# Kernel optimization log

Measured on AMD Instinct MI355X. Metric: run time of the kernel, lower is better.

The kernel has to match this reference:

```python
import jax, jax.numpy as jnp
import numpy as np

B, C_IN, T, IMG, P = 4, 3, 8, 224, 16
E, DEPTH, D_INNER, N_ST, DT_R, K = 384, 24, 768, 16, 24, 4
HP = IMG // P
NP_ = HP * HP          # 196 patches per frame
L = T * NP_            # 1568 tokens
EPS = 1e-5


def setup_inputs():
    key = jax.random.key(0)
    ks = jax.random.split(key, 24)
    r = lambda k, s, sc=0.02: jax.random.normal(k, s, jnp.float32) * sc
    inp = {
        "x": jax.random.normal(ks[0], (B, C_IN, T, IMG, IMG), jnp.float32),
        "patch_w": r(ks[1], (E, C_IN, 1, P, P)),
        "patch_b": jnp.zeros((E,), jnp.float32),
        "pos_embed": r(ks[2], (NP_, E)),
        "temporal_pos": r(ks[3], (T, E)),
        "imp_w1": r(ks[4], (E, E)),
        "imp_b1": jnp.zeros((E,), jnp.float32),
        "imp_w2": r(ks[5], (1, E)),
        "imp_b2": jnp.zeros((1,), jnp.float32),
        "in_w": r(ks[6], (DEPTH, 2 * D_INNER, E)),
        "out_w": r(ks[7], (DEPTH, E, D_INNER)),
        "norm_w": jnp.ones((DEPTH, E), jnp.float32),
        "norm_f_w": jnp.ones((E,), jnp.float32),
    }
    A_row = jnp.log(jnp.arange(1, N_ST + 1, dtype=jnp.float32))  # S4D-real init
    for i, sfx in enumerate(["", "_b"]):
        b = 8 + 4 * i
        inp["conv_w" + sfx] = r(ks[b], (DEPTH, D_INNER, K), 0.1)
        inp["conv_b" + sfx] = jnp.zeros((DEPTH, D_INNER), jnp.float32)
        inp["xp_w" + sfx] = r(ks[b + 1], (DEPTH, DT_R + 2 * N_ST, D_INNER))
        inp["dt_w" + sfx] = r(ks[b + 2], (DEPTH, D_INNER, DT_R), 0.01)
        inp["dt_b" + sfx] = jax.random.uniform(ks[b + 3], (DEPTH, D_INNER), jnp.float32, -4.6, -2.3)
        inp["A_log" + sfx] = jnp.tile(A_row, (DEPTH, D_INNER, 1))
        inp["D" + sfx] = jnp.ones((DEPTH, D_INNER), jnp.float32)
    return inp


def rmsnorm(x, w):
    x = x.astype(jnp.float32)
    return x * jax.lax.rsqrt(jnp.mean(x * x, axis=-1, keepdims=True) + EPS) * w


def causal_conv1d(x, w, b):
    # x: [B,L,D]; depthwise causal conv with kernel K
    xt = x.transpose(0, 2, 1)  # B D L
    y = jax.lax.conv_general_dilated(
        xt, w[:, None, :], (1,), [(K - 1, 0)],
        dimension_numbers=("NCH", "OIH", "NCH"), feature_group_count=D_INNER)
    return (y + b[None, :, None]).transpose(0, 2, 1)


def selective_scan(xt, dt, Bm, Cm, A, Dp):
    # xt,dt: [B,L,D]; Bm,Cm: [B,L,N]; A: [D,N]
    def step(h, ins):
        dt_t, x_t, B_t, C_t = ins  # [B,D],[B,D],[B,N],[B,N]
        h = h * jnp.exp(dt_t[..., None] * A) + (dt_t * x_t)[..., None] * B_t[:, None, :]
        return h, jnp.einsum('bdn,bn->bd', h, C_t)
    h0 = jnp.zeros((xt.shape[0], D_INNER, N_ST), xt.dtype)
    xs = (dt.transpose(1, 0, 2), xt.transpose(1, 0, 2),
          Bm.transpose(1, 0, 2), Cm.transpose(1, 0, 2))
    _, ys = jax.lax.scan(step, h0, xs)
    return ys.transpose(1, 0, 2) + xt * Dp


def mamba_dir(xc, z, cw, cb, xpw, dtw, dtb, Alog, Dp):
    xt = jax.nn.silu(causal_conv1d(xc, cw, cb))
    dbc = jnp.einsum('bld,ed->ble', xt, xpw)
    dt_low = dbc[..., :DT_R]
    Bm = dbc[..., DT_R:DT_R + N_ST]
    Cm = dbc[..., DT_R + N_ST:]
    dt = jax.nn.softplus(jnp.einsum('blr,dr->bld', dt_low, dtw) + dtb)
    y = selective_scan(xt, dt, Bm, Cm, -jnp.exp(Alog), Dp)
    return y * jax.nn.silu(z)


def mamba_block(h, p):
    xz = jnp.einsum('ble,fe->blf', h, p['in_w'])
    xc, z = xz[..., :D_INNER], xz[..., D_INNER:]
    yf = mamba_dir(xc, z, p['conv_w'], p['conv_b'], p['xp_w'], p['dt_w'], p['dt_b'], p['A_log'], p['D'])
    flip = lambda t: t[:, ::-1, :]
    yb = flip(mamba_dir(flip(xc), flip(z), p['conv_w_b'], p['conv_b_b'], p['xp_w_b'],
                        p['dt_w_b'], p['dt_b_b'], p['A_log_b'], p['D_b']))
    return jnp.einsum('bld,ed->ble', yf + yb, p['out_w'])


def _encoder(x, patch_w, patch_b, pos_embed, temporal_pos, imp_w1, imp_b1, imp_w2, imp_b2,
             in_w, out_w, norm_w, norm_f_w,
             conv_w, conv_b, xp_w, dt_w, dt_b, A_log, D,
             conv_w_b, conv_b_b, xp_w_b, dt_w_b, dt_b_b, A_log_b, D_b, mixer=mamba_block):
    Bn = x.shape[0]
    # PatchEmbed: Conv3d kernel (1,P,P) stride (1,P,P) == patchify + matmul
    xp = x.reshape(Bn, C_IN, T, HP, P, HP, P)
    xp = xp.transpose(0, 2, 3, 5, 1, 4, 6).reshape(Bn, T, NP_, C_IN * P * P)
    tok = xp @ patch_w.reshape(E, C_IN * P * P).T + patch_b  # [B,T,N,E]
    tok = tok + pos_embed[None, None] + temporal_pos[None, :, None, :]
    xseq = tok.reshape(Bn, L, E)
    # token importance gating
    h1 = jax.nn.relu(xseq @ imp_w1.T + imp_b1)
    logits = (h1 @ imp_w2.T + imp_b2)[..., 0]  # [B,L]
    xseq = xseq * jax.nn.sigmoid(logits)[..., None]
    stacked = {'in_w': in_w, 'out_w': out_w, 'norm_w': norm_w,
               'conv_w': conv_w, 'conv_b': conv_b, 'xp_w': xp_w, 'dt_w': dt_w,
               'dt_b': dt_b, 'A_log': A_log, 'D': D,
               'conv_w_b': conv_w_b, 'conv_b_b': conv_b_b, 'xp_w_b': xp_w_b,
               'dt_w_b': dt_w_b, 'dt_b_b': dt_b_b, 'A_log_b': A_log_b, 'D_b': D_b}

    def layer_fn(carry, p):
        hidden, residual = carry
        residual = (hidden + residual).astype(jnp.float32)  # fused add-norm, prenorm
        hn = rmsnorm(residual, p['norm_w'])
        hidden = mixer(hn, p)
        return (hidden, residual), None

    (hidden, residual), _ = jax.lax.scan(layer_fn, (xseq, jnp.zeros_like(xseq)), stacked)
    feats = rmsnorm(hidden + residual, norm_f_w)
    return feats, logits


def reference(x, patch_w, patch_b, pos_embed, temporal_pos, imp_w1, imp_b1, imp_w2, imp_b2,
              in_w, out_w, norm_w, norm_f_w,
              conv_w, conv_b, xp_w, dt_w, dt_b, A_log, D,
              conv_w_b, conv_b_b, xp_w_b, dt_w_b, dt_b_b, A_log_b, D_b):
    return _encoder(x, patch_w, patch_b, pos_embed, temporal_pos, imp_w1, imp_b1, imp_w2, imp_b2,
                    in_w, out_w, norm_w, norm_f_w,
                    conv_w, conv_b, xp_w, dt_w, dt_b, A_log, D,
                    conv_w_b, conv_b_b, xp_w_b, dt_w_b, dt_b_b, A_log_b, D_b)
```

## Files before the change

kernel.cpp:

```cpp
#include <hip/hip_runtime.h>
#include <hip/hip_bf16.h>

#define LL 1568
#define EE 384
#define DD 768
#define BB 4

typedef float f32x4 __attribute__((ext_vector_type(4)));
typedef unsigned short u16x2 __attribute__((ext_vector_type(2)));
typedef unsigned short u16x4 __attribute__((ext_vector_type(4)));
typedef unsigned short u16x8 __attribute__((ext_vector_type(8)));
typedef __bf16 bf16x8 __attribute__((ext_vector_type(8)));

__device__ inline unsigned short f2bf(float f) {
    unsigned int u = __builtin_bit_cast(unsigned int, f);
    u += 0x7fffu + ((u >> 16) & 1u);
    return (unsigned short)(u >> 16);
}
__device__ inline float bf2f(unsigned short u) {
    unsigned int v = ((unsigned int)u) << 16;
    return __builtin_bit_cast(float, v);
}
__device__ inline float silu_f(float v) { return v / (1.f + __expf(-v)); }
__device__ inline float exp2_f(float v) { return __builtin_amdgcn_exp2f(v); }

__global__ __launch_bounds__(256) void k_cvt(const float* __restrict__ src,
                                             unsigned short* __restrict__ dst, int n4) {
    int i = blockIdx.x * 256 + threadIdx.x;
    int stride = gridDim.x * 256;
    for (; i < n4; i += stride) {
        f32x4 v = *(const f32x4*)(src + (size_t)i * 4);
        u16x4 o;
#pragma unroll
        for (int j = 0; j < 4; j++) o[j] = f2bf(v[j]);
        *(u16x4*)(dst + (size_t)i * 4) = o;
    }
}

__global__ __launch_bounds__(256) void k_pad_xpw(const float* __restrict__ src,
                                                 unsigned short* __restrict__ dst) {
    const int total = 24 * 64 * 768;
    for (int i = blockIdx.x * 256 + threadIdx.x; i < total; i += gridDim.x * 256) {
        int l = i / (64 * 768);
        int r = (i / 768) % 64;
        int dcol = i % 768;
        dst[i] = (r < 56) ? f2bf(src[((size_t)l * 56 + r) * 768 + dcol]) : (unsigned short)0;
    }
}

__global__ __launch_bounds__(256) void k_pad_dtw(const float* __restrict__ src,
                                                 unsigned short* __restrict__ dst) {
    const int total = 24 * 768 * 32;
    for (int i = blockIdx.x * 256 + threadIdx.x; i < total; i += gridDim.x * 256) {
        int kk = i & 31;
        int nrow = i >> 5;
        dst[i] = (kk < 24) ? f2bf(src[(size_t)nrow * 24 + kk]) : (unsigned short)0;
    }
}

__global__ __launch_bounds__(256) void k_patch(const float* __restrict__ x,
                                               unsigned short* __restrict__ patches) {
    int bid = blockIdx.x;
    int b = bid / LL, rr = bid % LL, t = rr / 196, pp = rr % 196, hp = pp / 14, wp = pp % 14;
    for (int k = threadIdx.x; k < 768; k += 256) {
        int c = k >> 8, rem = k & 255, i = rem >> 4, j = rem & 15;
        patches[(size_t)bid * 768 + k] =
            f2bf(x[(((size_t)(b * 3 + c) * 8 + t) * 224 + hp * 16 + i) * 224 + wp * 16 + j]);
    }
}

template <int EPI, bool ASUM, bool OUTBF>
__global__ __launch_bounds__(256) void k_gemm(
    const unsigned short* __restrict__ A, const unsigned short* __restrict__ A2,
    const unsigned short* __restrict__ W, const unsigned short* __restrict__ W2,
    float* __restrict__ C, unsigned short* __restrict__ Cb, int K, int ldc,
    const float* __restrict__ bias, const float* __restrict__ bias2,
    const float* __restrict__ pos, const float* __restrict__ tpos) {
    const int tid = threadIdx.x;
    const int m0 = blockIdx.y * 128;
    const int n0 = blockIdx.x * 128;
    __shared__ unsigned short As[128 * 40];
    __shared__ unsigned short Ws[128 * 40];
    const int sr = tid >> 2;
    const int skc = tid & 3;

    const unsigned short* Wp = W;
    const float* biasp = bias;
    if constexpr (EPI == 3) {
        if (m0 >= 6272) { Wp = W2; biasp = bias2; }
    }

    f32x4 acc[4][4];
#pragma unroll
    for (int mi = 0; mi < 4; mi++)
#pragma unroll
        for (int ni = 0; ni < 4; ni++) acc[mi][ni] = (f32x4){0.f, 0.f, 0.f, 0.f};

    const int lane = tid & 63;
    const int wv = tid >> 6;
    const int wm = (wv & 1) << 6;
    const int wn = (wv >> 1) << 6;
    const int lr = lane & 15;
    const int kg = lane >> 4;

    u16x8 ar[2], wr_[2];
    auto loadT = [&](int kt) {
#pragma unroll
        for (int i = 0; i < 2; i++) {
            size_t ka = (size_t)(m0 + sr + 64 * i) * K + kt * 32 + skc * 8;
            u16x8 v = *(const u16x8*)(A + ka);
            if constexpr (ASUM) {
                u16x8 v2 = *(const u16x8*)(A2 + ka);
#pragma unroll
                for (int j = 0; j < 8; j++) v[j] = f2bf(bf2f(v[j]) + bf2f(v2[j]));
            }
            ar[i] = v;
            wr_[i] = *(const u16x8*)(Wp + (size_t)(n0 + sr + 64 * i) * K + kt * 32 + skc * 8);
        }
    };

    const int nK = K >> 5;
    loadT(0);
    for (int kt = 0; kt < nK; ++kt) {
#pragma unroll
        for (int i = 0; i < 2; i++) {
            *(u16x8*)&As[(sr + 64 * i) * 40 + skc * 8] = ar[i];
            *(u16x8*)&Ws[(sr + 64 * i) * 40 + skc * 8] = wr_[i];
        }
        __syncthreads();
        if (kt + 1 < nK) loadT(kt + 1);
        bf16x8 af[4], bfm[4];
#pragma unroll
        for (int mi = 0; mi < 4; mi++)
            af[mi] = *(const bf16x8*)&As[(wm + mi * 16 + lr) * 40 + kg * 8];
#pragma unroll
        for (int ni = 0; ni < 4; ni++)
            bfm[ni] = *(const bf16x8*)&Ws[(wn + ni * 16 + lr) * 40 + kg * 8];
#pragma unroll
        for (int mi = 0; mi < 4; mi++)
#pragma unroll
            for (int ni = 0; ni < 4; ni++)
                acc[mi][ni] = __builtin_amdgcn_mfma_f32_16x16x32_bf16(af[mi], bfm[ni], acc[mi][ni], 0, 0, 0);
        __syncthreads();
    }

#pragma unroll
    for (int mi = 0; mi < 4; mi++)
#pragma unroll
        for (int ni = 0; ni < 4; ni++)
#pragma unroll
            for (int j = 0; j < 4; j++) {
                int m = m0 + wm + mi * 16 + kg * 4 + j;
                int n = n0 + wn + ni * 16 + lr;
                float v = acc[mi][ni][j];
                if constexpr (EPI == 1) {
                    int rr = m % LL;
                    int t = rr / 196, p = rr % 196;
                    v += bias[n] + pos[p * EE + n] + tpos[t * EE + n];
                    C[(size_t)m * ldc + n] = v;
                    Cb[(size_t)m * ldc + n] = f2bf(v);
                } else if constexpr (EPI == 2) {
                    v += bias[n];
                    v = fmaxf(v, 0.f);
                    C[(size_t)m * ldc + n] = v;
                } else if constexpr (EPI == 3) {
                    v += biasp[n];
                    float sp = (v > 20.f) ? v : log1pf(__expf(v));
                    Cb[(size_t)m * ldc + n] = f2bf(sp);
                } else {
                    if constexpr (OUTBF)
                        Cb[(size_t)m * ldc + n] = f2bf(v);
                    else
                        C[(size_t)m * ldc + n] = v;
                }
            }
}

__global__ __launch_bounds__(64) void k_logits(const float* __restrict__ h1, const float* __restrict__ w2,
                                               const float* __restrict__ b2, float* __restrict__ xseq,
                                               float* __restrict__ logits_out) {
    int row = blockIdx.x;
    int lane = threadIdx.x;
    float acc = 0.f;
#pragma unroll
    for (int i = 0; i < 6; i++) {
        int e = lane + i * 64;
        acc += h1[(size_t)row * EE + e] * w2[e];
    }
#pragma unroll
    for (int off = 32; off >= 1; off >>= 1) acc += __shfl_xor(acc, off);
    float logit = acc + b2[0];
    if (lane == 0) logits_out[row] = logit;
    float sg = 1.f / (1.f + __expf(-logit));
#pragma unroll
    for (int i = 0; i < 6; i++) {
        int e = lane + i * 64;
        xseq[(size_t)row * EE + e] *= sg;
    }
}

template <bool OBF>
__global__ __launch_bounds__(256) void k_norm(const float* __restrict__ hidden, float* __restrict__ resid,
                                              const float* __restrict__ wn, float* __restrict__ outf,
                                              unsigned short* __restrict__ outb,
                                              int first, int writeResid) {
    int row = blockIdx.x * 4 + (threadIdx.x >> 6);
    int lane = threadIdx.x & 63;
    size_t base = (size_t)row * EE;
    float v[6];
    float ss = 0.f;
#pragma unroll
    for (int i = 0; i < 6; i++) {
        int e = lane + i * 64;
        float h = hidden[base + e];
        float r = first ? 0.f : resid[base + e];
        float s = h + r;
        v[i] = s;
        ss += s * s;
    }
#pragma unroll
    for (int off = 32; off >= 1; off >>= 1) ss += __shfl_xor(ss, off);
    if (writeResid) {
#pragma unroll
        for (int i = 0; i < 6; i++) resid[base + lane + i * 64] = v[i];
    }
    float sc = rsqrtf(ss * (1.f / 384.f) + 1e-5f);
#pragma unroll
    for (int i = 0; i < 6; i++) {
        int e = lane + i * 64;
        float o = v[i] * sc * wn[e];
        if constexpr (OBF)
            outb[base + e] = f2bf(o);
        else
            outf[base + e] = o;
    }
}

__global__ __launch_bounds__(256) void k_conv(
    const unsigned short* __restrict__ xz,
    const float* __restrict__ cw_f, const float* __restrict__ cb_f,
    const float* __restrict__ cw_b, const float* __restrict__ cb_b,
    unsigned short* __restrict__ xtb) {
    const int tid = threadIdx.x;
    if (tid >= 192) return;
    const int b = blockIdx.y, dir = blockIdx.z;
    const float* cw = dir ? cw_b : cw_f;
    const float* cb = dir ? cb_b : cb_f;
    const int o = tid % 96, tg = tid / 96;
    const int t0 = blockIdx.x * 16 + tg * 8;
    const int d0 = o * 8;
    const size_t xzb = (size_t)b * LL * 1536;
    const size_t obase = ((size_t)dir * BB + b) * LL;

    f32x4 wq[8];
    float bv[8];
#pragma unroll
    for (int j = 0; j < 8; j++) {
        wq[j] = *(const f32x4*)&cw[(d0 + j) * 4];
        bv[j] = cb[d0 + j];
    }

    auto loadrow = [&](int t) -> u16x8 {
        if (t < 0) return (u16x8){0, 0, 0, 0, 0, 0, 0, 0};
        int phys = dir ? (LL - 1 - t) : t;
        return *(const u16x8*)&xz[xzb + (size_t)phys * 1536 + d0];
    };

    float f0[8], f1[8], f2[8];
    u16x8 v;
    v = loadrow(t0 - 3);
#pragma unroll
    for (int j = 0; j < 8; j++) f0[j] = bf2f(v[j]);
    v = loadrow(t0 - 2);
#pragma unroll
    for (int j = 0; j < 8; j++) f1[j] = bf2f(v[j]);
    v = loadrow(t0 - 1);
#pragma unroll
    for (int j = 0; j < 8; j++) f2[j] = bf2f(v[j]);

    for (int s = 0; s < 8; ++s) {
        int t = t0 + s;
        v = loadrow(t);
        float f3[8];
        u16x8 outv;
#pragma unroll
        for (int j = 0; j < 8; j++) {
            f3[j] = bf2f(v[j]);
            float cv = wq[j][0] * f0[j] + wq[j][1] * f1[j] + wq[j][2] * f2[j] + wq[j][3] * f3[j] + bv[j];
            outv[j] = f2bf(silu_f(cv));
        }
        *(u16x8*)&xtb[(obase + t) * 768 + d0] = outv;
#pragma unroll
        for (int j = 0; j < 8; j++) { f0[j] = f1[j]; f1[j] = f2[j]; f2[j] = f3[j]; }
    }
}

__global__ __launch_bounds__(256) void k_dbc(
    const unsigned short* __restrict__ xtb,
    const unsigned short* __restrict__ xpwb_f, const unsigned short* __restrict__ xpwb_b,
    unsigned short* __restrict__ dtlow, float* __restrict__ Bm, float* __restrict__ Cm) {
    const int tid = threadIdx.x;
    const int m0 = blockIdx.x * 64;
    const unsigned short* W = (m0 >= 6272) ? xpwb_b : xpwb_f;
    __shared__ unsigned short As[64 * 40];
    __shared__ unsigned short Ws[64 * 40];
    const int sr = tid >> 2, skc = tid & 3;
    const int lane = tid & 63, wv = tid >> 6;
    const int lr = lane & 15, kg = lane >> 4;

    f32x4 acc[4];
#pragma unroll
    for (int mi = 0; mi < 4; mi++) acc[mi] = (f32x4){0.f, 0.f, 0.f, 0.f};

    u16x8 ar, wr_;
    auto loadT = [&](int kt) {
        ar = *(const u16x8*)(xtb + (size_t)(m0 + sr) * 768 + kt * 32 + skc * 8);
        wr_ = *(const u16x8*)(W + (size_t)sr * 768 + kt * 32 + skc * 8);
    };
    loadT(0);
    for (int kt = 0; kt < 24; ++kt) {
        *(u16x8*)&As[sr * 40 + skc * 8] = ar;
        *(u16x8*)&Ws[sr * 40 + skc * 8] = wr_;
        __syncthreads();
        if (kt + 1 < 24) loadT(kt + 1);
        bf16x8 bfm = *(const bf16x8*)&Ws[(wv * 16 + lr) * 40 + kg * 8];
#pragma unroll
        for (int mi = 0; mi < 4; mi++) {
            bf16x8 af = *(const bf16x8*)&As[(mi * 16 + lr) * 40 + kg * 8];
            acc[mi] = __builtin_amdgcn_mfma_f32_16x16x32_bf16(af, bfm, acc[mi], 0, 0, 0);
        }
        __syncthreads();
    }
#pragma unroll
    for (int mi = 0; mi < 4; mi++)
#pragma unroll
        for (int j = 0; j < 4; j++) {
            int row = m0 + mi * 16 + kg * 4 + j;
            int cc = wv * 16 + lr;
            float vv = acc[mi][j];
            if (cc < 24) dtlow[(size_t)row * 32 + cc] = f2bf(vv);
            else if (cc < 40) Bm[(size_t)row * 16 + (cc - 24)] = vv;
            else if (cc < 56) Cm[(size_t)row * 16 + (cc - 40)] = vv;
            else dtlow[(size_t)row * 32 + (cc - 32)] = 0;
        }
}

__global__ __launch_bounds__(512) void k_scan(
    const unsigned short* __restrict__ xtb, const unsigned short* __restrict__ dtb,
    const unsigned short* __restrict__ xz,
    const float* __restrict__ Bmat, const float* __restrict__ Cmat,
    const float* __restrict__ Alog_f, const float* __restrict__ Alog_b,
    const float* __restrict__ Dp_f, const float* __restrict__ Dp_b,
    unsigned short* __restrict__ ybuf) {
    const int tid = threadIdx.x;
    const int dl = tid & 15, c = tid >> 4;
    const int d = blockIdx.x * 16 + dl;
    const int b = blockIdx.y, dir = blockIdx.z;
    const float* Alog = dir ? Alog_b : Alog_f;
    const float* Dp = dir ? Dp_b : Dp_f;
    const int t0 = c * 49;

    __shared__ float Ssh[32][16][17];
    __shared__ float sdt_sh[32][16];

    float an[16];
#pragma unroll
    for (int n = 0; n < 16; n++) an[n] = -__expf(Alog[d * 16 + n]) * 1.44269504f;
    bool unif = (an[0] != 0.f);
#pragma unroll
    for (int n = 1; n < 16; n++) {
        float r = an[n] / an[0];
        unif = unif && (fabsf(r - (float)(n + 1)) < 1e-3f);
    }
    const float an0 = an[0];
    float Dd = Dp[d];

    const size_t dbase = ((size_t)dir * BB + b) * LL;
    const size_t rowb = dbase * 768 + d;

    float S[16];
#pragma unroll
    for (int n = 0; n < 16; n++) S[n] = 0.f;
    float sumdt = 0.f;

    for (int s = 0; s < 49; ++s) {
        int t = t0 + s;
        float xt = bf2f(xtb[rowb + (size_t)t * 768]);
        float dtv = bf2f(dtb[rowb + (size_t)t * 768]);
        sumdt += dtv;
        float dtx = dtv * xt;
        const f32x4* Bp = (const f32x4*)(Bmat + (dbase + t) * 16);
        f32x4 Bq[4] = {Bp[0], Bp[1], Bp[2], Bp[3]};
        if (unif) {
            float pw[16];
            pw[0] = exp2_f(dtv * an0);
            pw[1] = pw[0] * pw[0];
            pw[2] = pw[1] * pw[0];
            pw[3] = pw[1] * pw[1];
            pw[4] = pw[3] * pw[0];
            pw[5] = pw[3] * pw[1];
            pw[6] = pw[3] * pw[2];
            pw[7] = pw[3] * pw[3];
#pragma unroll
            for (int j = 0; j < 8; j++) pw[8 + j] = pw[7] * pw[j];
#pragma unroll
            for (int n = 0; n < 16; n++)
                S[n] = S[n] * pw[n] + dtx * Bq[n >> 2][n & 3];
        } else {
#pragma unroll
            for (int n = 0; n < 16; n++) {
                float e = exp2_f(dtv * an[n]);
                S[n] = S[n] * e + dtx * Bq[n >> 2][n & 3];
            }
        }
    }
#pragma unroll
    for (int n = 0; n < 16; n++) Ssh[c][dl][n] = S[n];
    sdt_sh[c][dl] = sumdt;
    __syncthreads();

    if (tid < 256) {
        int cdl = tid & 15, n2 = tid >> 4;
        float a_n = -__expf(Alog[(blockIdx.x * 16 + cdl) * 16 + n2]) * 1.44269504f;
        float H = 0.f;
#pragma unroll
        for (int c2 = 0; c2 < 32; c2++) {
            float P = exp2_f(a_n * sdt_sh[c2][cdl]);
            float tmp = Ssh[c2][cdl][n2];
            Ssh[c2][cdl][n2] = H;
            H = H * P + tmp;
        }
    }
    __syncthreads();

#pragma unroll
    for (int n = 0; n < 16; n++) S[n] = Ssh[c][dl][n];
    for (int s = 0; s < 49; ++s) {
        int t = t0 + s;
        float xt = bf2f(xtb[rowb + (size_t)t * 768]);
        float dtv = bf2f(dtb[rowb + (size_t)t * 768]);
        float dtx = dtv * xt;
        const f32x4* Bp = (const f32x4*)(Bmat + (dbase + t) * 16);
        f32x4 Bq[4] = {Bp[0], Bp[1], Bp[2], Bp[3]};
        const f32x4* Cp = (const f32x4*)(Cmat + (dbase + t) * 16);
        f32x4 Cq[4] = {Cp[0], Cp[1], Cp[2], Cp[3]};
        float y = 0.f;
        if (unif) {
            float pw[16];
            pw[0] = exp2_f(dtv * an0);
            pw[1] = pw[0] * pw[0];
            pw[2] = pw[1] * pw[0];
            pw[3] = pw[1] * pw[1];
            pw[4] = pw[3] * pw[0];
            pw[5] = pw[3] * pw[1];
            pw[6] = pw[3] * pw[2];
            pw[7] = pw[3] * pw[3];
#pragma unroll
            for (int j = 0; j < 8; j++) pw[8 + j] = pw[7] * pw[j];
#pragma unroll
            for (int n = 0; n < 16; n++) {
                S[n] = S[n] * pw[n] + dtx * Bq[n >> 2][n & 3];
                y += S[n] * Cq[n >> 2][n & 3];
            }
        } else {
#pragma unroll
            for (int n = 0; n < 16; n++) {
                float e = exp2_f(dtv * an[n]);
                S[n] = S[n] * e + dtx * Bq[n >> 2][n & 3];
                y += S[n] * Cq[n >> 2][n & 3];
            }
        }
        y += xt * Dd;
        int pt = dir ? (LL - 1 - t) : t;
        float zv = bf2f(xz[((size_t)b * LL + pt) * 1536 + 768 + d]);
        ybuf[rowb + (size_t)pt * 768] = f2bf(y * silu_f(zv));
    }
}

extern "C" void kernel_launch(void* const* d_in, const int* in_sizes, int n_in,
                              void* d_out, int out_size, void* d_ws, size_t ws_size,
                              hipStream_t stream) {
    const float* x        = (const float*)d_in[0];
    const float* patch_w  = (const float*)d_in[1];
    const float* patch_b  = (const float*)d_in[2];
    const float* pos_emb  = (const float*)d_in[3];
    const float* tpos     = (const float*)d_in[4];
    const float* imp_w1   = (const float*)d_in[5];
    const float* imp_b1   = (const float*)d_in[6];
    const float* imp_w2   = (const float*)d_in[7];
    const float* imp_b2   = (const float*)d_in[8];
    const float* in_w     = (const float*)d_in[9];
    const float* out_w    = (const float*)d_in[10];
    const float* norm_w   = (const float*)d_in[11];
    const float* norm_f_w = (const float*)d_in[12];
    const float* conv_w   = (const float*)d_in[13];
    const float* conv_b   = (const float*)d_in[14];
    const float* xp_w     = (const float*)d_in[15];
    const float* dt_w     = (const float*)d_in[16];
    const float* dt_b     = (const float*)d_in[17];
    const float* A_log    = (const float*)d_in[18];
    const float* Dp       = (const float*)d_in[19];
    const float* conv_w_b = (const float*)d_in[20];
    const float* conv_b_b = (const float*)d_in[21];
    const float* xp_w_b   = (const float*)d_in[22];
    const float* dt_w_b   = (const float*)d_in[23];
    const float* dt_b_b   = (const float*)d_in[24];
    const float* A_log_b  = (const float*)d_in[25];
    const float* D_b      = (const float*)d_in[26];

    float* out = (float*)d_out;
    float* logits_out = out + 2408448;

    char* wsb = (char*)d_ws;
    size_t off = 0;
    auto carve = [&](size_t bytes) { char* p = wsb + off; off += bytes; return p; };

    unsigned short* in_wb    = (unsigned short*)carve(28311552);
    unsigned short* out_wb   = (unsigned short*)carve(14155776);
    unsigned short* patch_wb = (unsigned short*)carve(589824);
    unsigned short* imp_w1b  = (unsigned short*)carve(294912);
    unsigned short* xpwb_f   = (unsigned short*)carve(2359296);
    unsigned short* xpwb_b   = (unsigned short*)carve(2359296);
    unsigned short* dtwb_f   = (unsigned short*)carve(1179648);
    unsigned short* dtwb_b   = (unsigned short*)carve(1179648);
    float*          hidden   = (float*)carve(9633792);
    float*          resid    = (float*)carve(9633792);
    unsigned short* hn       = (unsigned short*)carve(4816896);
    unsigned short* xzb      = (unsigned short*)carve(19267584);
    unsigned short* xtb      = (unsigned short*)carve(19267584);
    unsigned short* g_dt     = (unsigned short*)carve(19267584);
    unsigned short* dtlow    = (unsigned short*)carve(802816);
    float*          Bm       = (float*)carve(802816);
    float*          Cm       = (float*)carve(802816);
    unsigned short* ybuf     = (unsigned short*)carve(19267584);

    float*          h1       = (float*)xtb;
    unsigned short* hidb     = (unsigned short*)g_dt;
    unsigned short* patches  = (unsigned short*)ybuf;

    k_cvt<<<2048, 256, 0, stream>>>(in_w, in_wb, 3538944);
    k_cvt<<<2048, 256, 0, stream>>>(out_w, out_wb, 1769472);
    k_cvt<<<288, 256, 0, stream>>>(patch_w, patch_wb, 73728);
    k_cvt<<<144, 256, 0, stream>>>(imp_w1, imp_w1b, 36864);
    k_pad_xpw<<<1024, 256, 0, stream>>>(xp_w, xpwb_f);
    k_pad_xpw<<<1024, 256, 0, stream>>>(xp_w_b, xpwb_b);
    k_pad_dtw<<<1024, 256, 0, stream>>>(dt_w, dtwb_f);
    k_pad_dtw<<<1024, 256, 0, stream>>>(dt_w_b, dtwb_b);

    k_patch<<<6272, 256, 0, stream>>>(x, patches);
    k_gemm<1, false, false><<<dim3(3, 49), 256, 0, stream>>>(patches, nullptr, patch_wb, nullptr,
                                                             hidden, hidb, 768, 384,
                                                             patch_b, nullptr, pos_emb, tpos);
    k_gemm<2, false, false><<<dim3(3, 49), 256, 0, stream>>>(hidb, nullptr, imp_w1b, nullptr,
                                                             h1, nullptr, 384, 384,
                                                             imp_b1, nullptr, nullptr, nullptr);
    k_logits<<<6272, 64, 0, stream>>>(h1, imp_w2, imp_b2, hidden, logits_out);

    for (int l = 0; l < 24; ++l) {
        k_norm<true><<<1568, 256, 0, stream>>>(hidden, resid, norm_w + l * 384, nullptr, hn,
                                               (l == 0) ? 1 : 0, 1);
        k_gemm<0, false, true><<<dim3(12, 49), 256, 0, stream>>>(hn, nullptr, in_wb + (size_t)l * 589824,
                                                                 nullptr, nullptr, xzb, 384, 1536,
                                                                 nullptr, nullptr, nullptr, nullptr);
        k_conv<<<dim3(98, 4, 2), 256, 0, stream>>>(xzb, conv_w + l * 3072, conv_b + l * 768,
                                                   conv_w_b + l * 3072, conv_b_b + l * 768, xtb);
        k_dbc<<<196, 256, 0, stream>>>(xtb, xpwb_f + (size_t)l * 49152, xpwb_b + (size_t)l * 49152,
                                       dtlow, Bm, Cm);
        k_gemm<3, false, true><<<dim3(6, 98), 256, 0, stream>>>(dtlow, nullptr,
                                                                dtwb_f + (size_t)l * 24576,
                                                                dtwb_b + (size_t)l * 24576,
                                                                nullptr, g_dt, 32, 768,
                                                                dt_b + l * 768, dt_b_b + l * 768,
                                                                nullptr, nullptr);
        k_scan<<<dim3(48, 4, 2), 512, 0, stream>>>(
            xtb, g_dt, xzb, Bm, Cm,
            A_log + l * 12288, A_log_b + l * 12288,
            Dp + l * 768, D_b + l * 768,
            ybuf);
        k_gemm<0, true, false><<<dim3(3, 49), 256, 0, stream>>>(ybuf, ybuf + 4816896,
                                                                out_wb + (size_t)l * 294912, nullptr,
                                                                hidden, nullptr, 768, 384,
                                                                nullptr, nullptr, nullptr, nullptr);
    }
    k_norm<false><<<1568, 256, 0, stream>>>(hidden, resid, norm_f_w, out, nullptr, 0, 0);
}
```

Baseline: 5.287 ms.

## Store conv output and dt transposed so scan reads contiguous time vectors

The conv kernel now also writes a channel-major (d, time) copy of its output, and the dt projection GEMM is run with swapped operands so softplus(dt) comes out in the same transposed layout. The scan then loads 8 consecutive timesteps per vector load instead of making strided per-timestep scalar loads. The chunking changes from 32 chunks of 49 steps to 49 chunks of 32 steps, with 784 threads per block. The cost is an extra transposed write from conv, an extra 19MB buffer, two GEMM launches instead of one, and a larger block size with more registers held per thread.

```diff
diff --git a/kernel.cpp b/kernel.cpp
--- a/kernel.cpp
+++ b/kernel.cpp
@@ -72,9 +72,9 @@
 template <int EPI, bool ASUM, bool OUTBF>
 __global__ __launch_bounds__(256) void k_gemm(
     const unsigned short* __restrict__ A, const unsigned short* __restrict__ A2,
-    const unsigned short* __restrict__ W, const unsigned short* __restrict__ W2,
+    const unsigned short* __restrict__ W,
     float* __restrict__ C, unsigned short* __restrict__ Cb, int K, int ldc,
-    const float* __restrict__ bias, const float* __restrict__ bias2,
+    const float* __restrict__ bias,
     const float* __restrict__ pos, const float* __restrict__ tpos) {
     const int tid = threadIdx.x;
     const int m0 = blockIdx.y * 128;
@@ -84,12 +84,6 @@
     const int sr = tid >> 2;
     const int skc = tid & 3;
 
-    const unsigned short* Wp = W;
-    const float* biasp = bias;
-    if constexpr (EPI == 3) {
-        if (m0 >= 6272) { Wp = W2; biasp = bias2; }
-    }
-
     f32x4 acc[4][4];
 #pragma unroll
     for (int mi = 0; mi < 4; mi++)
@@ -115,7 +109,7 @@
                 for (int j = 0; j < 8; j++) v[j] = f2bf(bf2f(v[j]) + bf2f(v2[j]));
             }
             ar[i] = v;
-            wr_[i] = *(const u16x8*)(Wp + (size_t)(n0 + sr + 64 * i) * K + kt * 32 + skc * 8);
+            wr_[i] = *(const u16x8*)(W + (size_t)(n0 + sr + 64 * i) * K + kt * 32 + skc * 8);
         }
     };
 
@@ -164,7 +158,7 @@
                     v = fmaxf(v, 0.f);
                     C[(size_t)m * ldc + n] = v;
                 } else if constexpr (EPI == 3) {
-                    v += biasp[n];
+                    v += bias[m];
                     float sp = (v > 20.f) ? v : log1pf(__expf(v));
                     Cb[(size_t)m * ldc + n] = f2bf(sp);
                 } else {
@@ -240,7 +234,7 @@
     const unsigned short* __restrict__ xz,
     const float* __restrict__ cw_f, const float* __restrict__ cb_f,
     const float* __restrict__ cw_b, const float* __restrict__ cb_b,
-    unsigned short* __restrict__ xtb) {
+    unsigned short* __restrict__ xtb, unsigned short* __restrict__ xtT) {
     const int tid = threadIdx.x;
     if (tid >= 192) return;
     const int b = blockIdx.y, dir = blockIdx.z;
@@ -278,6 +272,8 @@
 #pragma unroll
     for (int j = 0; j < 8; j++) f2[j] = bf2f(v[j]);
 
+    u16x8 tvj[8];
+#pragma unroll
     for (int s = 0; s < 8; ++s) {
         int t = t0 + s;
         v = loadrow(t);
@@ -287,11 +283,18 @@
         for (int j = 0; j < 8; j++) {
             f3[j] = bf2f(v[j]);
             float cv = wq[j][0] * f0[j] + wq[j][1] * f1[j] + wq[j][2] * f2[j] + wq[j][3] * f3[j] + bv[j];
-            outv[j] = f2bf(silu_f(cv));
+            unsigned short ob = f2bf(silu_f(cv));
+            outv[j] = ob;
+            tvj[j][s] = ob;
         }
         *(u16x8*)&xtb[(obase + t) * 768 + d0] = outv;
 #pragma unroll
         for (int j = 0; j < 8; j++) { f0[j] = f1[j]; f1[j] = f2[j]; f2[j] = f3[j]; }
+    }
+#pragma unroll
+    for (int j = 0; j < 8; j++) {
+        size_t tr = ((size_t)dir * 768 + (d0 + j)) * 6272 + (size_t)b * 1568 + t0;
+        *(u16x8*)&xtT[tr] = tvj[j];
     }
 }
 
@@ -345,8 +348,8 @@
         }
 }
 
-__global__ __launch_bounds__(512) void k_scan(
-    const unsigned short* __restrict__ xtb, const unsigned short* __restrict__ dtb,
+__global__ __launch_bounds__(784) void k_scan(
+    const unsigned short* __restrict__ xtT, const unsigned short* __restrict__ dtT,
     const unsigned short* __restrict__ xz,
     const float* __restrict__ Bmat, const float* __restrict__ Cmat,
     const float* __restrict__ Alog_f, const float* __restrict__ Alog_b,
@@ -358,10 +361,10 @@
     const int b = blockIdx.y, dir = blockIdx.z;
     const float* Alog = dir ? Alog_b : Alog_f;
     const float* Dp = dir ? Dp_b : Dp_f;
-    const int t0 = c * 49;
-
-    __shared__ float Ssh[32][16][17];
-    __shared__ float sdt_sh[32][16];
+    const int t0 = c * 32;
+
+    __shared__ float Ssh[49][16][17];
+    __shared__ float sdt_sh[49][16];
 
     float an[16];
 #pragma unroll
@@ -376,41 +379,46 @@
     float Dd = Dp[d];
 
     const size_t dbase = ((size_t)dir * BB + b) * LL;
-    const size_t rowb = dbase * 768 + d;
+    const size_t trow = ((size_t)dir * 768 + d) * 6272 + (size_t)b * 1568;
 
     float S[16];
 #pragma unroll
     for (int n = 0; n < 16; n++) S[n] = 0.f;
     float sumdt = 0.f;
 
-    for (int s = 0; s < 49; ++s) {
-        int t = t0 + s;
-        float xt = bf2f(xtb[rowb + (size_t)t * 768]);
-        float dtv = bf2f(dtb[rowb + (size_t)t * 768]);
-        sumdt += dtv;
-        float dtx = dtv * xt;
-        const f32x4* Bp = (const f32x4*)(Bmat + (dbase + t) * 16);
-        f32x4 Bq[4] = {Bp[0], Bp[1], Bp[2], Bp[3]};
-        if (unif) {
-            float pw[16];
-            pw[0] = exp2_f(dtv * an0);
-            pw[1] = pw[0] * pw[0];
-            pw[2] = pw[1] * pw[0];
-            pw[3] = pw[1] * pw[1];
-            pw[4] = pw[3] * pw[0];
-            pw[5] = pw[3] * pw[1];
-            pw[6] = pw[3] * pw[2];
-            pw[7] = pw[3] * pw[3];
-#pragma unroll
-            for (int j = 0; j < 8; j++) pw[8 + j] = pw[7] * pw[j];
-#pragma unroll
-            for (int n = 0; n < 16; n++)
-                S[n] = S[n] * pw[n] + dtx * Bq[n >> 2][n & 3];
-        } else {
-#pragma unroll
-            for (int n = 0; n < 16; n++) {
-                float e = exp2_f(dtv * an[n]);
-                S[n] = S[n] * e + dtx * Bq[n >> 2][n & 3];
+    for (int s8 = 0; s8 < 4; ++s8) {
+        u16x8 xv = *(const u16x8*)&xtT[trow + t0 + s8 * 8];
+        u16x8 dv = *(const u16x8*)&dtT[trow + t0 + s8 * 8];
+#pragma unroll
+        for (int j = 0; j < 8; ++j) {
+            int t = t0 + s8 * 8 + j;
+            float xt = bf2f(xv[j]);
+            float dtv = bf2f(dv[j]);
+            sumdt += dtv;
+            float dtx = dtv * xt;
+            const f32x4* Bp = (const f32x4*)(Bmat + (dbase + t) * 16);
+            f32x4 Bq[4] = {Bp[0], Bp[1], Bp[2], Bp[3]};
+            if (unif) {
+                float pw[16];
+                pw[0] = exp2_f(dtv * an0);
+                pw[1] = pw[0] * pw[0];
+                pw[2] = pw[1] * pw[0];
+                pw[3] = pw[1] * pw[1];
+                pw[4] = pw[3] * pw[0];
+                pw[5] = pw[3] * pw[1];
+                pw[6] = pw[3] * pw[2];
+                pw[7] = pw[3] * pw[3];
+#pragma unroll
+                for (int q = 0; q < 8; q++) pw[8 + q] = pw[7] * pw[q];
+#pragma unroll
+                for (int n = 0; n < 16; n++)
+                    S[n] = S[n] * pw[n] + dtx * Bq[n >> 2][n & 3];
+            } else {
+#pragma unroll
+                for (int n = 0; n < 16; n++) {
+                    float e = exp2_f(dtv * an[n]);
+                    S[n] = S[n] * e + dtx * Bq[n >> 2][n & 3];
+                }
             }
         }
     }
@@ -423,8 +431,7 @@
         int cdl = tid & 15, n2 = tid >> 4;
         float a_n = -__expf(Alog[(blockIdx.x * 16 + cdl) * 16 + n2]) * 1.44269504f;
         float H = 0.f;
-#pragma unroll
-        for (int c2 = 0; c2 < 32; c2++) {
+        for (int c2 = 0; c2 < 49; c2++) {
             float P = exp2_f(a_n * sdt_sh[c2][cdl]);
             float tmp = Ssh[c2][cdl][n2];
             Ssh[c2][cdl][n2] = H;
@@ -435,45 +442,50 @@
 
 #pragma unroll
     for (int n = 0; n < 16; n++) S[n] = Ssh[c][dl][n];
-    for (int s = 0; s < 49; ++s) {
-        int t = t0 + s;
-        float xt = bf2f(xtb[rowb + (size_t)t * 768]);
-        float dtv = bf2f(dtb[rowb + (size_t)t * 768]);
-        float dtx = dtv * xt;
-        const f32x4* Bp = (const f32x4*)(Bmat + (dbase + t) * 16);
-        f32x4 Bq[4] = {Bp[0], Bp[1], Bp[2], Bp[3]};
-        const f32x4* Cp = (const f32x4*)(Cmat + (dbase + t) * 16);
-        f32x4 Cq[4] = {Cp[0], Cp[1], Cp[2], Cp[3]};
-        float y = 0.f;
-        if (unif) {
-            float pw[16];
-            pw[0] = exp2_f(dtv * an0);
-            pw[1] = pw[0] * pw[0];
-            pw[2] = pw[1] * pw[0];
-            pw[3] = pw[1] * pw[1];
-            pw[4] = pw[3] * pw[0];
-            pw[5] = pw[3] * pw[1];
-            pw[6] = pw[3] * pw[2];
-            pw[7] = pw[3] * pw[3];
-#pragma unroll
-            for (int j = 0; j < 8; j++) pw[8 + j] = pw[7] * pw[j];
-#pragma unroll
-            for (int n = 0; n < 16; n++) {
-                S[n] = S[n] * pw[n] + dtx * Bq[n >> 2][n & 3];
-                y += S[n] * Cq[n >> 2][n & 3];
+    for (int s8 = 0; s8 < 4; ++s8) {
+        u16x8 xv = *(const u16x8*)&xtT[trow + t0 + s8 * 8];
+        u16x8 dv = *(const u16x8*)&dtT[trow + t0 + s8 * 8];
+#pragma unroll
+        for (int j = 0; j < 8; ++j) {
+            int t = t0 + s8 * 8 + j;
+            float xt = bf2f(xv[j]);
+            float dtv = bf2f(dv[j]);
+            float dtx = dtv * xt;
+            const f32x4* Bp = (const f32x4*)(Bmat + (dbase + t) * 16);
+            f32x4 Bq[4] = {Bp[0], Bp[1], Bp[2], Bp[3]};
+            const f32x4* Cp = (const f32x4*)(Cmat + (dbase + t) * 16);
+            f32x4 Cq[4] = {Cp[0], Cp[1], Cp[2], Cp[3]};
+            float y = 0.f;
+            if (unif) {
+                float pw[16];
+                pw[0] = exp2_f(dtv * an0);
+                pw[1] = pw[0] * pw[0];
+                pw[2] = pw[1] * pw[0];
+                pw[3] = pw[1] * pw[1];
+                pw[4] = pw[3] * pw[0];
+                pw[5] = pw[3] * pw[1];
+                pw[6] = pw[3] * pw[2];
+                pw[7] = pw[3] * pw[3];
+#pragma unroll
+                for (int q = 0; q < 8; q++) pw[8 + q] = pw[7] * pw[q];
+#pragma unroll
+                for (int n = 0; n < 16; n++) {
+                    S[n] = S[n] * pw[n] + dtx * Bq[n >> 2][n & 3];
+                    y += S[n] * Cq[n >> 2][n & 3];
+                }
+            } else {
+#pragma unroll
+                for (int n = 0; n < 16; n++) {
+                    float e = exp2_f(dtv * an[n]);
+                    S[n] = S[n] * e + dtx * Bq[n >> 2][n & 3];
+                    y += S[n] * Cq[n >> 2][n & 3];
+                }
             }
-        } else {
-#pragma unroll
-            for (int n = 0; n < 16; n++) {
-                float e = exp2_f(dtv * an[n]);
-                S[n] = S[n] * e + dtx * Bq[n >> 2][n & 3];
-                y += S[n] * Cq[n >> 2][n & 3];
-            }
-        }
-        y += xt * Dd;
-        int pt = dir ? (LL - 1 - t) : t;
-        float zv = bf2f(xz[((size_t)b * LL + pt) * 1536 + 768 + d]);
-        ybuf[rowb + (size_t)pt * 768] = f2bf(y * silu_f(zv));
+            y += xt * Dd;
+            int pt = dir ? (LL - 1 - t) : t;
+            float zv = bf2f(xz[((size_t)b * LL + pt) * 1536 + 768 + d]);
+            ybuf[(dbase + pt) * 768 + d] = f2bf(y * silu_f(zv));
+        }
     }
 }
 
@@ -528,14 +540,15 @@
     unsigned short* hn       = (unsigned short*)carve(4816896);
     unsigned short* xzb      = (unsigned short*)carve(19267584);
     unsigned short* xtb      = (unsigned short*)carve(19267584);
-    unsigned short* g_dt     = (unsigned short*)carve(19267584);
+    unsigned short* xtT      = (unsigned short*)carve(19267584);
+    unsigned short* g_dtT    = (unsigned short*)carve(19267584);
     unsigned short* dtlow    = (unsigned short*)carve(802816);
     float*          Bm       = (float*)carve(802816);
     float*          Cm       = (float*)carve(802816);
     unsigned short* ybuf     = (unsigned short*)carve(19267584);
 
     float*          h1       = (float*)xtb;
-    unsigned short* hidb     = (unsigned short*)g_dt;
+    unsigned short* hidb     = (unsigned short*)g_dtT;
     unsigned short* patches  = (unsigned short*)ybuf;
 
     k_cvt<<<2048, 256, 0, stream>>>(in_w, in_wb, 3538944);
@@ -548,39 +561,40 @@
     k_pad_dtw<<<1024, 256, 0, stream>>>(dt_w_b, dtwb_b);
 
     k_patch<<<6272, 256, 0, stream>>>(x, patches);
-    k_gemm<1, false, false><<<dim3(3, 49), 256, 0, stream>>>(patches, nullptr, patch_wb, nullptr,
+    k_gemm<1, false, false><<<dim3(3, 49), 256, 0, stream>>>(patches, nullptr, patch_wb,
                                                              hidden, hidb, 768, 384,
-                                                             patch_b, nullptr, pos_emb, tpos);
-    k_gemm<2, false, false><<<dim3(3, 49), 256, 0, stream>>>(hidb, nullptr, imp_w1b, nullptr,
+                                                             patch_b, pos_emb, tpos);
+    k_gemm<2, false, false><<<dim3(3, 49), 256, 0, stream>>>(hidb, nullptr, imp_w1b,
                                                              h1, nullptr, 384, 384,
-                                                             imp_b1, nullptr, nullptr, nullptr);
+                                                             imp_b1, nullptr, nullptr);
     k_logits<<<6272, 64, 0, stream>>>(h1, imp_w2, imp_b2, hidden, logits_out);
 
     for (int l = 0; l < 24; ++l) {
         k_norm<true><<<1568, 256, 0, stream>>>(hidden, resid, norm_w + l * 384, nullptr, hn,
                                                (l == 0) ? 1 : 0, 1);
         k_gemm<0, false, true><<<dim3(12, 49), 256, 0, stream>>>(hn, nullptr, in_wb + (size_t)l * 589824,
-                                                                 nullptr, nullptr, xzb, 384, 1536,
-                                                                 nullptr, nullptr, nullptr, nullptr);
+                                                                 nullptr, xzb, 384, 1536,
+                                                                 nullptr, nullptr, nullptr);
         k_conv<<<dim3(98, 4, 2), 256, 0, stream>>>(xzb, conv_w + l * 3072, conv_b + l * 768,
-                                                   conv_w_b + l * 3072, conv_b_b + l * 768, xtb);
+                                                   conv_w_b + l * 3072, conv_b_b + l * 768, xtb, xtT);
         k_dbc<<<196, 256, 0, stream>>>(xtb, xpwb_f + (size_t)l * 49152, xpwb_b + (size_t)l * 49152,
                                        dtlow, Bm, Cm);
-        k_gemm<3, false, true><<<dim3(6, 98), 256, 0, stream>>>(dtlow, nullptr,
-                                                                dtwb_f + (size_t)l * 24576,
-                                                                dtwb_b + (size_t)l * 24576,
-                                                                nullptr, g_dt, 32, 768,
-                                                                dt_b + l * 768, dt_b_b + l * 768,
-                                                                nullptr, nullptr);
-        k_scan<<<dim3(48, 4, 2), 512, 0, stream>>>(
-            xtb, g_dt, xzb, Bm, Cm,
+        k_gemm<3, false, true><<<dim3(49, 6), 256, 0, stream>>>(dtwb_f + (size_t)l * 24576, nullptr,
+                                                                dtlow, nullptr, g_dtT, 32, 6272,
+                                                                dt_b + l * 768, nullptr, nullptr);
+        k_gemm<3, false, true><<<dim3(49, 6), 256, 0, stream>>>(dtwb_b + (size_t)l * 24576, nullptr,
+                                                                dtlow + (size_t)6272 * 32, nullptr,
+                                                                g_dtT + (size_t)768 * 6272, 32, 6272,
+                                                                dt_b_b + l * 768, nullptr, nullptr);
+        k_scan<<<dim3(48, 4, 2), 784, 0, stream>>>(
+            xtT, g_dtT, xzb, Bm, Cm,
             A_log + l * 12288, A_log_b + l * 12288,
             Dp + l * 768, D_b + l * 768,
             ybuf);
         k_gemm<0, true, false><<<dim3(3, 49), 256, 0, stream>>>(ybuf, ybuf + 4816896,
-                                                                out_wb + (size_t)l * 294912, nullptr,
+                                                                out_wb + (size_t)l * 294912,
                                                                 hidden, nullptr, 768, 384,
-                                                                nullptr, nullptr, nullptr, nullptr);
+                                                                nullptr, nullptr, nullptr);
     }
     k_norm<false><<<1568, 256, 0, stream>>>(hidden, resid, norm_f_w, out, nullptr, 0, 0);
 }
```

Measured after the change: 6.469 ms. 22.4% more time.
